# Kernel optimization log

Hardware: AMD Instinct MI355X
Metric: run time of the kernel (lower is better)

The kernel has to match this reference:

```python
import jax, jax.numpy as jnp
import numpy as np

N = 50000      # nodes
E = 800000     # edges (avg degree 16)
IN = 256       # input feature dim
HID = 128      # hidden dim
H = 4          # heads
C = HID // H   # per-head dim = 32
L = 3          # layers


def setup_inputs() -> dict:
    key = jax.random.key(0)
    ks = jax.random.split(key, 16)
    s = 0.02
    f32 = jnp.float32
    inp = {
        "x": jax.random.normal(ks[0], (N, IN), f32),
        "edge_index": jax.random.randint(ks[1], (2, E), 0, N, dtype=jnp.int32),
        "edge_attr": jax.random.normal(ks[2], (E, 1), f32),
        "Wi": jax.random.normal(ks[3], (IN, HID), f32) * s,
        "bi": jnp.zeros((HID,), f32),
        "Wq": jax.random.normal(ks[4], (L, HID, HID), f32) * s,
        "bq": jnp.zeros((L, HID), f32),
        "Wk": jax.random.normal(ks[5], (L, HID, HID), f32) * s,
        "bk": jnp.zeros((L, HID), f32),
        "Wv": jax.random.normal(ks[6], (L, HID, HID), f32) * s,
        "bv": jnp.zeros((L, HID), f32),
        "We": jax.random.normal(ks[7], (L, 1, HID), f32) * s,      # lin_edge, no bias
        "Wskip": jax.random.normal(ks[8], (L, HID, HID), f32) * s,
        "bskip": jnp.zeros((L, HID), f32),
        "Wbeta": jax.random.normal(ks[9], (L, 3 * HID, 1), f32) * s,  # lin_beta, no bias
        "ln_g": jnp.ones((L, HID), f32),
        "ln_b": jnp.zeros((L, HID), f32),
    }
    return inp


def _layer_norm(x, g, b, eps=1e-5):
    mu = jnp.mean(x, axis=-1, keepdims=True)
    var = jnp.var(x, axis=-1, keepdims=True)
    return (x - mu) * jax.lax.rsqrt(var + eps) * g + b


def _transformer_conv(h, src, dst, edge_attr, Wq, bq, Wk, bk, Wv, bv, We, Wskip, bskip, Wbeta):
    # node-level projections [N, HID]
    q = h @ Wq + bq
    k = h @ Wk + bk
    v = h @ Wv + bv
    e = edge_attr @ We                       # [E, HID] edge embedding
    # per-edge gathered features [E, H, C]
    qi = q[dst].reshape(E, H, C)
    kj = (k[src] + e).reshape(E, H, C)
    vj = (v[src] + e).reshape(E, H, C)
    # attention logits [E, H]
    alpha = jnp.sum(qi * kj, axis=-1) / np.sqrt(C)
    # segment softmax over destination node
    amax = jax.ops.segment_max(alpha, dst, num_segments=N)   # [N, H]
    ex = jnp.exp(alpha - amax[dst])
    denom = jax.ops.segment_sum(ex, dst, num_segments=N)     # [N, H]
    attn = ex / (denom[dst] + 1e-16)                         # [E, H]
    # scatter-add aggregation -> [N, H, C] -> concat heads [N, HID]
    out = jax.ops.segment_sum(attn[..., None] * vj, dst, num_segments=N).reshape(N, HID)
    # gated skip (beta=True, root_weight=True)
    x_r = h @ Wskip + bskip
    beta = jax.nn.sigmoid(jnp.concatenate([out, x_r, out - x_r], axis=-1) @ Wbeta)  # [N, 1]
    return beta * x_r + (1.0 - beta) * out


def reference(x, edge_index, edge_attr, Wi, bi, Wq, bq, Wk, bk, Wv, bv, We, Wskip, bskip, Wbeta, ln_g, ln_b):
    src = edge_index[0]
    dst = edge_index[1]
    h = x @ Wi + bi
    for l in range(L):
        res = h
        h = _transformer_conv(h, src, dst, edge_attr,
                              Wq[l], bq[l], Wk[l], bk[l], Wv[l], bv[l],
                              We[l], Wskip[l], bskip[l], Wbeta[l])
        h = jax.nn.gelu(h, approximate=False)
        h = _layer_norm(h + res, ln_g[l], ln_b[l])
        # dropout: eval mode -> identity
    return h
```

## Files before the change

kernel.cpp:

```cpp
#include <hip/hip_runtime.h>
#include <math.h>

#define NNODES 50000
#define NEDGES 800000
#define DIN 256
#define DHID 128

typedef __attribute__((ext_vector_type(8))) short short8;
typedef __attribute__((ext_vector_type(4))) float f32x4;
typedef __attribute__((ext_vector_type(2))) float f32x2;

__device__ __forceinline__ unsigned short f2bf(float f) {
    unsigned u = __builtin_bit_cast(unsigned, f);
    u += 0x7fffu + ((u >> 16) & 1u);
    return (unsigned short)(u >> 16);
}
__device__ __forceinline__ float bf2f(unsigned short s) {
    return __builtin_bit_cast(float, (unsigned)s << 16);
}
__device__ __forceinline__ unsigned packbf(float a, float b) {
    return (unsigned)f2bf(a) | ((unsigned)f2bf(b) << 16);
}

__global__ __launch_bounds__(256) void k_hist(const int* __restrict__ dst, int* __restrict__ counts) {
    int e = blockIdx.x * 256 + threadIdx.x;
    if (e < NEDGES) atomicAdd(&counts[dst[e]], 1);
}

__global__ __launch_bounds__(256) void k_scan_block(const int* __restrict__ in, int* __restrict__ out,
                                                    int* __restrict__ partials, int n) {
    __shared__ int sh[256];
    int tid = threadIdx.x;
    int i = blockIdx.x * 256 + tid;
    int vv = (i < n) ? in[i] : 0;
    sh[tid] = vv;
    __syncthreads();
    for (int off = 1; off < 256; off <<= 1) {
        int t = (tid >= off) ? sh[tid - off] : 0;
        __syncthreads();
        sh[tid] += t;
        __syncthreads();
    }
    if (i < n) out[i] = sh[tid];
    if (tid == 255) partials[blockIdx.x] = sh[255];
}

__global__ __launch_bounds__(256) void k_scan_partials(int* __restrict__ partials, int nb) {
    __shared__ int sh[256];
    int tid = threadIdx.x;
    int vv = (tid < nb) ? partials[tid] : 0;
    sh[tid] = vv;
    __syncthreads();
    for (int off = 1; off < 256; off <<= 1) {
        int t = (tid >= off) ? sh[tid - off] : 0;
        __syncthreads();
        sh[tid] += t;
        __syncthreads();
    }
    if (tid < nb) partials[tid] = sh[tid];
}

__global__ __launch_bounds__(256) void k_apply(const int* __restrict__ partials, int* __restrict__ row_ptr, int n) {
    int i = blockIdx.x * 256 + threadIdx.x;
    if (i < n) {
        int add = blockIdx.x ? partials[blockIdx.x - 1] : 0;
        row_ptr[i + 1] += add;
    }
    if (i == 0) row_ptr[0] = 0;
}

__global__ __launch_bounds__(256) void k_scatter(const int* __restrict__ src, const int* __restrict__ dst,
                                                 const float* __restrict__ ea, const int* __restrict__ row_ptr,
                                                 int* __restrict__ fill, int2* __restrict__ esrc) {
    int e = blockIdx.x * 256 + threadIdx.x;
    if (e < NEDGES) {
        int d = dst[e];
        int old = atomicSub(&fill[d], 1);
        int pos = row_ptr[d] + old - 1;
        esrc[pos] = make_int2(src[e], __float_as_int(ea[e]));
    }
}

__global__ __launch_bounds__(256) void prep_w(const float* __restrict__ Wi, const float* __restrict__ Wq,
                                              const float* __restrict__ Wk, const float* __restrict__ Wv,
                                              const float* __restrict__ Ws, unsigned short* __restrict__ Wit,
                                              unsigned short* __restrict__ Wt3) {
    int idx = blockIdx.x * 256 + threadIdx.x;
    if (idx < DHID * DIN) {
        int n = idx >> 8, kk = idx & 255;
        Wit[idx] = f2bf(Wi[kk * DHID + n]);
    }
    int idx2 = idx - DHID * DIN;
    if (idx2 >= 0 && idx2 < 3 * 512 * DHID) {
        int l = idx2 / (512 * DHID);
        int rem = idx2 - l * 512 * DHID;
        int r = rem >> 7;
        int kk = rem & 127;
        int sel = r >> 7, rl = r & 127;
        const float* srcm = sel == 0 ? Wq : sel == 1 ? Wk : sel == 2 ? Wv : Ws;
        Wt3[idx2] = f2bf(srcm[l * DHID * DHID + kk * DHID + rl]);
    }
}

__global__ __launch_bounds__(256) void gemm_in(const float* __restrict__ A, const unsigned short* __restrict__ Wt,
                                               const float* __restrict__ bias, unsigned* __restrict__ h32, int M) {
    __shared__ short As[128 * 128];
    const int tid = threadIdx.x;
    const int lane = tid & 63;
    const int wid = tid >> 6;
    const int row0 = blockIdx.x * 128;
    const int wr = (wid & 1) * 64;
    const int wc = (wid >> 1) * 64;
    f32x4 acc[4][4] = {};
    const int srow = tid >> 1;
    const int sk = (tid & 1) * 64;
    const int grow = min(row0 + srow, M - 1);
    for (int kt = 0; kt < 2; ++kt) {
        const float* ap = A + (size_t)grow * DIN + kt * 128 + sk;
#pragma unroll
        for (int i = 0; i < 8; ++i) {
            float4 f0 = *(const float4*)(ap + i * 8);
            float4 f1 = *(const float4*)(ap + i * 8 + 4);
            short8 s;
            s[0] = f2bf(f0.x); s[1] = f2bf(f0.y); s[2] = f2bf(f0.z); s[3] = f2bf(f0.w);
            s[4] = f2bf(f1.x); s[5] = f2bf(f1.y); s[6] = f2bf(f1.z); s[7] = f2bf(f1.w);
            int g = (sk >> 3) + i;
            *(short8*)(&As[srow * 128 + ((g ^ (srow & 7)) << 3)]) = s;
        }
        __syncthreads();
#pragma unroll
        for (int ks = 0; ks < 4; ++ks) {
            short8 a[4], b[4];
#pragma unroll
            for (int m = 0; m < 4; ++m) {
                int r = wr + m * 16 + (lane & 15);
                int g = ks * 4 + (lane >> 4);
                a[m] = *(const short8*)(&As[r * 128 + ((g ^ (r & 7)) << 3)]);
            }
#pragma unroll
            for (int n = 0; n < 4; ++n) {
                int c = wc + n * 16 + (lane & 15);
                b[n] = *(const short8*)(Wt + (size_t)c * DIN + kt * 128 + ks * 32 + (lane >> 4) * 8);
            }
#pragma unroll
            for (int m = 0; m < 4; ++m)
#pragma unroll
                for (int n = 0; n < 4; ++n)
                    acc[m][n] = __builtin_amdgcn_mfma_f32_16x16x32_bf16(a[m], b[n], acc[m][n], 0, 0, 0);
        }
        __syncthreads();
    }
    float* my = ((float*)As) + wid * 1024;
    float bb[4];
#pragma unroll
    for (int n = 0; n < 4; ++n) bb[n] = bias[wc + n * 16 + (lane & 15)];
    const int rr = lane >> 2;
    const int cb = lane & 3;
#pragma unroll
    for (int m = 0; m < 4; ++m) {
#pragma unroll
        for (int n = 0; n < 4; ++n) {
            int lc = n * 16 + (lane & 15);
#pragma unroll
            for (int j = 0; j < 4; ++j) {
                int row = (lane >> 4) * 4 + j;
                my[row * 64 + (((lc >> 2) ^ (row & 7)) << 2) + (lc & 3)] = acc[m][n][j] + bb[n];
            }
        }
        float vals[16];
#pragma unroll
        for (int s = 0; s < 4; ++s) {
            int gx = (cb * 4 + s) ^ (rr & 7);
            f32x4 t4 = *(const f32x4*)(my + rr * 64 + gx * 4);
            vals[s * 4 + 0] = t4.x; vals[s * 4 + 1] = t4.y; vals[s * 4 + 2] = t4.z; vals[s * 4 + 3] = t4.w;
        }
        int grow2 = row0 + wr + m * 16 + rr;
        if (grow2 < M) {
            unsigned pk[8];
#pragma unroll
            for (int d = 0; d < 8; ++d) pk[d] = packbf(vals[2 * d], vals[2 * d + 1]);
            unsigned* op = h32 + (size_t)grow2 * 64 + (wc >> 1) + cb * 8;
            *(uint4*)op = make_uint4(pk[0], pk[1], pk[2], pk[3]);
            *(uint4*)(op + 4) = make_uint4(pk[4], pk[5], pk[6], pk[7]);
        }
    }
}

__global__ __launch_bounds__(512) void gemm_qkvs(const unsigned short* __restrict__ A,
                                                 const unsigned short* __restrict__ Wt, const float* __restrict__ bq,
                                                 const float* __restrict__ bk, const float* __restrict__ bv,
                                                 const float* __restrict__ bs, unsigned* __restrict__ q32,
                                                 unsigned* __restrict__ kv, unsigned* __restrict__ xr32, int M) {
    __shared__ short As[128 * 128];
    const int tid = threadIdx.x;
    const int lane = tid & 63;
    const int wid = tid >> 6;
    const int row0 = blockIdx.x * 128;
    const int sel = wid >> 2;
    const int wr = (wid & 1) * 64;
    const int wc = ((wid >> 1) & 1) * 64;
    f32x4 acc0[4][4] = {}, acc1[4][4] = {};
    {
        const int srow = tid >> 2;
        const int sk = (tid & 3) * 32;
        const int grow = min(row0 + srow, M - 1);
        const unsigned short* ap = A + (size_t)grow * DHID + sk;
#pragma unroll
        for (int i = 0; i < 4; ++i) {
            short8 s = *(const short8*)(ap + i * 8);
            int g = (sk >> 3) + i;
            *(short8*)(&As[srow * 128 + ((g ^ (srow & 7)) << 3)]) = s;
        }
    }
    __syncthreads();
    const int b0base = sel ? 128 : 0;
    const int b1base = sel ? 256 : 384;
#pragma unroll
    for (int ks = 0; ks < 4; ++ks) {
        short8 a[4], b0[4], b1[4];
#pragma unroll
        for (int m = 0; m < 4; ++m) {
            int r = wr + m * 16 + (lane & 15);
            int g = ks * 4 + (lane >> 4);
            a[m] = *(const short8*)(&As[r * 128 + ((g ^ (r & 7)) << 3)]);
        }
#pragma unroll
        for (int n = 0; n < 4; ++n) {
            int rb = wc + n * 16 + (lane & 15);
            b0[n] = *(const short8*)(Wt + (size_t)(b0base + rb) * DHID + ks * 32 + (lane >> 4) * 8);
            b1[n] = *(const short8*)(Wt + (size_t)(b1base + rb) * DHID + ks * 32 + (lane >> 4) * 8);
        }
#pragma unroll
        for (int m = 0; m < 4; ++m)
#pragma unroll
            for (int n = 0; n < 4; ++n) {
                acc0[m][n] = __builtin_amdgcn_mfma_f32_16x16x32_bf16(a[m], b0[n], acc0[m][n], 0, 0, 0);
                acc1[m][n] = __builtin_amdgcn_mfma_f32_16x16x32_bf16(a[m], b1[n], acc1[m][n], 0, 0, 0);
            }
    }
    __syncthreads();
    float* my = ((float*)As) + wid * 1024;
    const float* bias0 = sel ? bk : bq;
    const float* bias1 = sel ? bv : bs;
    float bb0[4], bb1[4];
#pragma unroll
    for (int n = 0; n < 4; ++n) {
        int c = wc + n * 16 + (lane & 15);
        bb0[n] = bias0[c];
        bb1[n] = bias1[c];
    }
    const int rr = lane >> 2;
    const int cb = lane & 3;
#pragma unroll
    for (int m = 0; m < 4; ++m) {
        float vals0[16], vals1[16];
#pragma unroll
        for (int n = 0; n < 4; ++n) {
            int lc = n * 16 + (lane & 15);
#pragma unroll
            for (int j = 0; j < 4; ++j) {
                int row = (lane >> 4) * 4 + j;
                my[row * 64 + (((lc >> 2) ^ (row & 7)) << 2) + (lc & 3)] = acc0[m][n][j] + bb0[n];
            }
        }
#pragma unroll
        for (int s = 0; s < 4; ++s) {
            int gx = (cb * 4 + s) ^ (rr & 7);
            f32x4 t4 = *(const f32x4*)(my + rr * 64 + gx * 4);
            vals0[s * 4 + 0] = t4.x; vals0[s * 4 + 1] = t4.y; vals0[s * 4 + 2] = t4.z; vals0[s * 4 + 3] = t4.w;
        }
#pragma unroll
        for (int n = 0; n < 4; ++n) {
            int lc = n * 16 + (lane & 15);
#pragma unroll
            for (int j = 0; j < 4; ++j) {
                int row = (lane >> 4) * 4 + j;
                my[row * 64 + (((lc >> 2) ^ (row & 7)) << 2) + (lc & 3)] = acc1[m][n][j] + bb1[n];
            }
        }
#pragma unroll
        for (int s = 0; s < 4; ++s) {
            int gx = (cb * 4 + s) ^ (rr & 7);
            f32x4 t4 = *(const f32x4*)(my + rr * 64 + gx * 4);
            vals1[s * 4 + 0] = t4.x; vals1[s * 4 + 1] = t4.y; vals1[s * 4 + 2] = t4.z; vals1[s * 4 + 3] = t4.w;
        }
        int grow2 = row0 + wr + m * 16 + rr;
        if (grow2 < M) {
            size_t obase = (size_t)grow2 * 64 + (wc >> 1) + cb * 8;
            if (sel == 0) {
                unsigned p0[8], p1[8];
#pragma unroll
                for (int d = 0; d < 8; ++d) {
                    p0[d] = packbf(vals0[2 * d], vals0[2 * d + 1]);
                    p1[d] = packbf(vals1[2 * d], vals1[2 * d + 1]);
                }
                *(uint4*)(q32 + obase) = make_uint4(p0[0], p0[1], p0[2], p0[3]);
                *(uint4*)(q32 + obase + 4) = make_uint4(p0[4], p0[5], p0[6], p0[7]);
                *(uint4*)(xr32 + obase) = make_uint4(p1[0], p1[1], p1[2], p1[3]);
                *(uint4*)(xr32 + obase + 4) = make_uint4(p1[4], p1[5], p1[6], p1[7]);
            } else {
                unsigned pk[8];
#pragma unroll
                for (int d = 0; d < 8; ++d) {
                    unsigned u = (unsigned)__builtin_amdgcn_cvt_pk_fp8_f32(vals0[2 * d], vals0[2 * d + 1], 0, false);
                    u = (unsigned)__builtin_amdgcn_cvt_pk_fp8_f32(vals1[2 * d], vals1[2 * d + 1], (int)u, true);
                    pk[d] = u;
                }
                *(uint4*)(kv + obase) = make_uint4(pk[0], pk[1], pk[2], pk[3]);
                *(uint4*)(kv + obase + 4) = make_uint4(pk[4], pk[5], pk[6], pk[7]);
            }
        }
    }
}

__global__ __launch_bounds__(256) void node_attn_fuse(const unsigned* __restrict__ q32,
                                                      const unsigned* __restrict__ kv, const int2* __restrict__ esrc,
                                                      const float* __restrict__ We, const int* __restrict__ row_ptr,
                                                      const unsigned* __restrict__ xr32, const unsigned* res32,
                                                      const float* __restrict__ Wb, const float* __restrict__ lng,
                                                      const float* __restrict__ lnb, unsigned* houtb, float* houtf) {
    __shared__ float sh_o[4][128];
    const int tid = threadIdx.x;
    const int wv = tid >> 6;
    const int lane = tid & 63;
    const int wid = blockIdx.x * 4 + wv;
    if (wid >= NNODES) return;
    const int ln = lane & 15;
    const int g = lane >> 4;
    const int base = row_ptr[wid], end = row_ptr[wid + 1];
    const float SC = 0.25505654047688565f;
    const float THR = 8.0f;

    float qv[8], wev[8];
    {
        uint4 qw = *(const uint4*)(q32 + (size_t)wid * 64 + 4 * ln);
#pragma unroll
        for (int t = 0; t < 4; ++t) {
            unsigned u = ((const unsigned*)&qw)[t];
            qv[2 * t] = bf2f((unsigned short)u) * SC;
            qv[2 * t + 1] = bf2f((unsigned short)(u >> 16)) * SC;
        }
        float4 wlo = *(const float4*)(We + 8 * ln);
        float4 whi = *(const float4*)(We + 8 * ln + 4);
        wev[0] = wlo.x; wev[1] = wlo.y; wev[2] = wlo.z; wev[3] = wlo.w;
        wev[4] = whi.x; wev[5] = whi.y; wev[6] = whi.z; wev[7] = whi.w;
    }
    float qwe = 0.f;
#pragma unroll
    for (int i = 0; i < 8; ++i) qwe = fmaf(qv[i], wev[i], qwe);
    qwe += __shfl_xor(qwe, 1);
    qwe += __shfl_xor(qwe, 2);

    float m = -1e30f, sden = 0.f, tacc = 0.f;
    float acc[8] = {};
    const unsigned* kvp = kv + 4 * ln;

    for (int cbse = base; cbse < end; cbse += 64) {
        int cnt = min(end - cbse, 64);
        int s_l = 0;
        float a_l = 0.f;
        if (lane < cnt) {
            int2 sa = esrc[cbse + lane];
            s_l = sa.x;
            a_l = __int_as_float(sa.y);
        }
        int jmax = (cnt + 3) >> 2;
        for (int j = 0; j < jmax; ++j) {
            int slot = j * 4 + g;
            bool valid = slot < cnt;
            int sN = __shfl(s_l, slot);
            float av = __shfl(a_l, slot);
            if (!valid) sN = 0;
            uint4 kvw = *(const uint4*)(kvp + (size_t)sN * 64);
            float vj[8];
            float p = 0.f;
#pragma unroll
            for (int t = 0; t < 4; ++t) {
                unsigned u = ((const unsigned*)&kvw)[t];
                f32x2 kk = __builtin_amdgcn_cvt_pk_f32_fp8((int)u, false);
                f32x2 vv = __builtin_amdgcn_cvt_pk_f32_fp8((int)u, true);
                p = fmaf(qv[2 * t], kk.x, p);
                p = fmaf(qv[2 * t + 1], kk.y, p);
                vj[2 * t] = vv.x;
                vj[2 * t + 1] = vv.y;
            }
            p += __shfl_xor(p, 1);
            p += __shfl_xor(p, 2);
            p = fmaf(av, qwe, p);
            p = valid ? p : -3e38f;
            if (__all(p - m <= THR)) {
                float wgt = exp2f(p - m);
                sden += wgt;
                tacc = fmaf(wgt, av, tacc);
#pragma unroll
                for (int i = 0; i < 8; ++i) acc[i] = fmaf(wgt, vj[i], acc[i]);
            } else {
                float mn = fmaxf(m, p);
                float wgt = exp2f(p - mn);
                float sc = exp2f(m - mn);
                sden = fmaf(sden, sc, wgt);
                tacc = fmaf(tacc, sc, wgt * av);
#pragma unroll
                for (int i = 0; i < 8; ++i) acc[i] = fmaf(acc[i], sc, wgt * vj[i]);
                m = mn;
            }
        }
    }

#pragma unroll
    for (int off = 16; off <= 32; off <<= 1) {
        float m_o = __shfl_xor(m, off);
        float sden_o = __shfl_xor(sden, off);
        float t_o = __shfl_xor(tacc, off);
        float mn = fmaxf(m, m_o);
        float sa = exp2f(m - mn), sb = exp2f(m_o - mn);
        sden = sden * sa + sden_o * sb;
        tacc = tacc * sa + t_o * sb;
#pragma unroll
        for (int i = 0; i < 8; ++i) acc[i] = acc[i] * sa + __shfl_xor(acc[i], off) * sb;
        m = mn;
    }
    float rden = 1.f / (sden + 1e-16f);
    if (g == 0) {
#pragma unroll
        for (int i = 0; i < 8; ++i) sh_o[wv][8 * ln + i] = fmaf(tacc, wev[i], acc[i]) * rden;
    }
    __asm__ volatile("s_waitcnt lgkmcnt(0)" ::: "memory");

    const int c0 = 2 * lane;
    const float2 ov0v = *(const float2*)(&sh_o[wv][c0]);
    float o0 = ov0v.x, o1 = ov0v.y;
    const unsigned xw = xr32[(size_t)wid * 64 + lane];
    const float x0 = bf2f((unsigned short)xw), x1 = bf2f((unsigned short)(xw >> 16));
    const float2 w0 = *(const float2*)(Wb + c0);
    const float2 w1 = *(const float2*)(Wb + 128 + c0);
    const float2 w2 = *(const float2*)(Wb + 256 + c0);
    float bl = o0 * w0.x + o1 * w0.y + x0 * w1.x + x1 * w1.y + (o0 - x0) * w2.x + (o1 - x1) * w2.y;
#pragma unroll
    for (int off = 32; off; off >>= 1) bl += __shfl_xor(bl, off);
    float beta = 1.f / (1.f + __expf(-bl));
    float g0 = beta * x0 + (1.f - beta) * o0;
    float g1 = beta * x1 + (1.f - beta) * o1;
    g0 = 0.5f * g0 * (1.f + erff(g0 * 0.70710678118654752f));
    g1 = 0.5f * g1 * (1.f + erff(g1 * 0.70710678118654752f));
    const unsigned rw = res32[(size_t)wid * 64 + lane];
    float t0 = g0 + bf2f((unsigned short)rw);
    float t1 = g1 + bf2f((unsigned short)(rw >> 16));
    float su = t0 + t1, sq = t0 * t0 + t1 * t1;
#pragma unroll
    for (int off = 32; off; off >>= 1) {
        su += __shfl_xor(su, off);
        sq += __shfl_xor(sq, off);
    }
    float mu = su * (1.f / 128.f);
    float var = sq * (1.f / 128.f) - mu * mu;
    float inv = rsqrtf(var + 1e-5f);
    const float2 gv = *(const float2*)(lng + c0);
    const float2 bv2 = *(const float2*)(lnb + c0);
    float ovx = (t0 - mu) * inv * gv.x + bv2.x;
    float ovy = (t1 - mu) * inv * gv.y + bv2.y;
    if (houtf) {
        *(float2*)(houtf + (size_t)wid * 128 + c0) = make_float2(ovx, ovy);
    } else {
        houtb[(size_t)wid * 64 + lane] = packbf(ovx, ovy);
    }
}

extern "C" void kernel_launch(void* const* d_in, const int* in_sizes, int n_in, void* d_out, int out_size,
                              void* d_ws, size_t ws_size, hipStream_t stream) {
    const float* x = (const float*)d_in[0];
    const int* ei = (const int*)d_in[1];
    const float* ea = (const float*)d_in[2];
    const float* Wi = (const float*)d_in[3];
    const float* bi = (const float*)d_in[4];
    const float* Wq = (const float*)d_in[5];
    const float* bq = (const float*)d_in[6];
    const float* Wk = (const float*)d_in[7];
    const float* bk = (const float*)d_in[8];
    const float* Wv = (const float*)d_in[9];
    const float* bv = (const float*)d_in[10];
    const float* We = (const float*)d_in[11];
    const float* Wskip = (const float*)d_in[12];
    const float* bskip = (const float*)d_in[13];
    const float* Wbeta = (const float*)d_in[14];
    const float* lng = (const float*)d_in[15];
    const float* lnb = (const float*)d_in[16];

    const int* srcp = ei;
    const int* dstp = ei + NEDGES;

    char* p = (char*)d_ws;
    auto alloc = [&](size_t bytes) {
        void* r = (void*)p;
        p += (bytes + 255) & ~(size_t)255;
        return r;
    };
    unsigned* h32 = (unsigned*)alloc((size_t)NNODES * 64 * 4);
    unsigned* q32 = (unsigned*)alloc((size_t)NNODES * 64 * 4);
    unsigned* xr32 = (unsigned*)alloc((size_t)NNODES * 64 * 4);
    unsigned* kv = (unsigned*)alloc((size_t)NNODES * 64 * 4);
    unsigned short* Wit = (unsigned short*)alloc((size_t)DHID * DIN * 2);
    unsigned short* Wt3 = (unsigned short*)alloc((size_t)3 * 512 * DHID * 2);
    int* counts = (int*)alloc((size_t)NNODES * 4);
    int* row_ptr = (int*)alloc((size_t)(NNODES + 1) * 4);
    int2* esrc = (int2*)alloc((size_t)NEDGES * 8);
    int* partials = (int*)alloc(256 * 4);

    const int EB = (NEDGES + 255) / 256;
    const int NB = (NNODES + 255) / 256;
    const int GB = (NNODES + 127) / 128;
    const int WB = (NNODES + 3) / 4;
    const int PB = (DHID * DIN + 3 * 512 * DHID + 255) / 256;

    prep_w<<<PB, 256, 0, stream>>>(Wi, Wq, Wk, Wv, Wskip, Wit, Wt3);

    hipMemsetAsync(counts, 0, (size_t)NNODES * 4, stream);
    k_hist<<<EB, 256, 0, stream>>>(dstp, counts);
    k_scan_block<<<NB, 256, 0, stream>>>(counts, row_ptr + 1, partials, NNODES);
    k_scan_partials<<<1, 256, 0, stream>>>(partials, NB);
    k_apply<<<NB, 256, 0, stream>>>(partials, row_ptr, NNODES);
    k_scatter<<<EB, 256, 0, stream>>>(srcp, dstp, ea, row_ptr, counts, esrc);

    gemm_in<<<GB, 256, 0, stream>>>(x, Wit, bi, h32, NNODES);

    for (int l = 0; l < 3; ++l) {
        const size_t bo = (size_t)l * 128;
        gemm_qkvs<<<GB, 512, 0, stream>>>((const unsigned short*)h32, Wt3 + (size_t)l * 512 * DHID, bq + bo, bk + bo,
                                          bv + bo, bskip + bo, q32, kv, xr32, NNODES);
        node_attn_fuse<<<WB, 256, 0, stream>>>(q32, kv, esrc, We + bo, row_ptr, xr32, h32,
                                               Wbeta + (size_t)l * 384, lng + bo, lnb + bo, h32,
                                               (l == 2) ? (float*)d_out : nullptr);
    }
}
```

Before: 376.2 us.

## Process 8 edges per wave with prefetched KV rows and DPP reductions

The attention kernel now assigns 8 lanes per edge, so each lane handles 16 channels and the wave covers 8 edges per iteration instead of 4. Edge metadata is staged in shared memory, and the next edge's KV row is prefetched one iteration ahead to hide gather latency. Cross-lane reductions use DPP moves in place of some shuffles. The separate partial-scan kernel is folded into the apply kernel, which drops one launch. The trade-off is more registers per lane (16 accumulators plus prefetch buffers), which may lower occupancy, and low-degree nodes waste more lanes per iteration.

```diff
diff --git a/kernel.cpp b/kernel.cpp
--- a/kernel.cpp
+++ b/kernel.cpp
@@ -20,6 +20,12 @@
 }
 __device__ __forceinline__ unsigned packbf(float a, float b) {
     return (unsigned)f2bf(a) | ((unsigned)f2bf(b) << 16);
+}
+__device__ __forceinline__ float dpp_xor1(float x) {
+    return __builtin_bit_cast(float, __builtin_amdgcn_update_dpp(0, __builtin_bit_cast(int, x), 0xB1, 0xF, 0xF, true));
+}
+__device__ __forceinline__ float dpp_xor8(float x) {
+    return __builtin_bit_cast(float, __builtin_amdgcn_update_dpp(0, __builtin_bit_cast(int, x), 0x128, 0xF, 0xF, true));
 }
 
 __global__ __launch_bounds__(256) void k_hist(const int* __restrict__ dst, int* __restrict__ counts) {
@@ -45,7 +51,8 @@
     if (tid == 255) partials[blockIdx.x] = sh[255];
 }
 
-__global__ __launch_bounds__(256) void k_scan_partials(int* __restrict__ partials, int nb) {
+__global__ __launch_bounds__(256) void k_apply2(const int* __restrict__ partials, int* __restrict__ row_ptr, int n,
+                                                int nb) {
     __shared__ int sh[256];
     int tid = threadIdx.x;
     int vv = (tid < nb) ? partials[tid] : 0;
@@ -57,13 +64,9 @@
         sh[tid] += t;
         __syncthreads();
     }
-    if (tid < nb) partials[tid] = sh[tid];
-}
-
-__global__ __launch_bounds__(256) void k_apply(const int* __restrict__ partials, int* __restrict__ row_ptr, int n) {
-    int i = blockIdx.x * 256 + threadIdx.x;
+    int i = blockIdx.x * 256 + tid;
     if (i < n) {
-        int add = blockIdx.x ? partials[blockIdx.x - 1] : 0;
+        int add = blockIdx.x ? sh[blockIdx.x - 1] : 0;
         row_ptr[i + 1] += add;
     }
     if (i == 0) row_ptr[0] = 0;
@@ -320,72 +323,81 @@
                                                       const float* __restrict__ Wb, const float* __restrict__ lng,
                                                       const float* __restrict__ lnb, unsigned* houtb, float* houtf) {
     __shared__ float sh_o[4][128];
+    __shared__ int2 sh_meta[4][64];
     const int tid = threadIdx.x;
     const int wv = tid >> 6;
     const int lane = tid & 63;
     const int wid = blockIdx.x * 4 + wv;
     if (wid >= NNODES) return;
-    const int ln = lane & 15;
-    const int g = lane >> 4;
+    const int ln = lane & 7;
+    const int g = lane >> 3;
     const int base = row_ptr[wid], end = row_ptr[wid + 1];
     const float SC = 0.25505654047688565f;
     const float THR = 8.0f;
 
-    float qv[8], wev[8];
+    float qv[16];
     {
-        uint4 qw = *(const uint4*)(q32 + (size_t)wid * 64 + 4 * ln);
+        uint4 qa = *(const uint4*)(q32 + (size_t)wid * 64 + 8 * ln);
+        uint4 qb = *(const uint4*)(q32 + (size_t)wid * 64 + 8 * ln + 4);
+        unsigned qd[8] = {qa.x, qa.y, qa.z, qa.w, qb.x, qb.y, qb.z, qb.w};
+#pragma unroll
+        for (int t = 0; t < 8; ++t) {
+            qv[2 * t] = bf2f((unsigned short)qd[t]) * SC;
+            qv[2 * t + 1] = bf2f((unsigned short)(qd[t] >> 16)) * SC;
+        }
+    }
+    float qwe;
+    {
+        float s = 0.f;
 #pragma unroll
         for (int t = 0; t < 4; ++t) {
-            unsigned u = ((const unsigned*)&qw)[t];
-            qv[2 * t] = bf2f((unsigned short)u) * SC;
-            qv[2 * t + 1] = bf2f((unsigned short)(u >> 16)) * SC;
-        }
-        float4 wlo = *(const float4*)(We + 8 * ln);
-        float4 whi = *(const float4*)(We + 8 * ln + 4);
-        wev[0] = wlo.x; wev[1] = wlo.y; wev[2] = wlo.z; wev[3] = wlo.w;
-        wev[4] = whi.x; wev[5] = whi.y; wev[6] = whi.z; wev[7] = whi.w;
-    }
-    float qwe = 0.f;
-#pragma unroll
-    for (int i = 0; i < 8; ++i) qwe = fmaf(qv[i], wev[i], qwe);
-    qwe += __shfl_xor(qwe, 1);
-    qwe += __shfl_xor(qwe, 2);
+            float4 w4 = *(const float4*)(We + 16 * ln + 4 * t);
+            s = fmaf(qv[4 * t], w4.x, s);
+            s = fmaf(qv[4 * t + 1], w4.y, s);
+            s = fmaf(qv[4 * t + 2], w4.z, s);
+            s = fmaf(qv[4 * t + 3], w4.w, s);
+        }
+        qwe = s + dpp_xor1(s);
+    }
 
     float m = -1e30f, sden = 0.f, tacc = 0.f;
-    float acc[8] = {};
-    const unsigned* kvp = kv + 4 * ln;
+    float acc[16] = {};
+    const unsigned* kvp = kv + 8 * ln;
 
     for (int cbse = base; cbse < end; cbse += 64) {
         int cnt = min(end - cbse, 64);
-        int s_l = 0;
-        float a_l = 0.f;
-        if (lane < cnt) {
-            int2 sa = esrc[cbse + lane];
-            s_l = sa.x;
-            a_l = __int_as_float(sa.y);
-        }
-        int jmax = (cnt + 3) >> 2;
+        int2 me = (lane < cnt) ? esrc[cbse + lane] : make_int2(0, 0);
+        sh_meta[wv][lane] = me;
+        __asm__ volatile("s_waitcnt lgkmcnt(0)" ::: "memory");
+        int jmax = (cnt + 7) >> 3;
+        int2 mc = sh_meta[wv][g];
+        const unsigned* rowp = kvp + (size_t)mc.x * 64;
+        uint4 ka = *(const uint4*)rowp;
+        uint4 kb = *(const uint4*)(rowp + 4);
         for (int j = 0; j < jmax; ++j) {
-            int slot = j * 4 + g;
-            bool valid = slot < cnt;
-            int sN = __shfl(s_l, slot);
-            float av = __shfl(a_l, slot);
-            if (!valid) sN = 0;
-            uint4 kvw = *(const uint4*)(kvp + (size_t)sN * 64);
-            float vj[8];
+            bool more = (j + 1 < jmax);
+            int2 mn_ = sh_meta[wv][(((j + 1) << 3) + g) & 63];
+            uint4 ka1 = ka, kb1 = kb;
+            if (more) {
+                const unsigned* rowp1 = kvp + (size_t)mn_.x * 64;
+                ka1 = *(const uint4*)rowp1;
+                kb1 = *(const uint4*)(rowp1 + 4);
+            }
+            bool valid = ((j << 3) + g) < cnt;
+            float av = __int_as_float(mc.y);
+            unsigned kd[8] = {ka.x, ka.y, ka.z, ka.w, kb.x, kb.y, kb.z, kb.w};
+            float vj[16];
             float p = 0.f;
 #pragma unroll
-            for (int t = 0; t < 4; ++t) {
-                unsigned u = ((const unsigned*)&kvw)[t];
-                f32x2 kk = __builtin_amdgcn_cvt_pk_f32_fp8((int)u, false);
-                f32x2 vv = __builtin_amdgcn_cvt_pk_f32_fp8((int)u, true);
+            for (int t = 0; t < 8; ++t) {
+                f32x2 kk = __builtin_amdgcn_cvt_pk_f32_fp8((int)kd[t], false);
+                f32x2 vvv = __builtin_amdgcn_cvt_pk_f32_fp8((int)kd[t], true);
                 p = fmaf(qv[2 * t], kk.x, p);
                 p = fmaf(qv[2 * t + 1], kk.y, p);
-                vj[2 * t] = vv.x;
-                vj[2 * t + 1] = vv.y;
-            }
-            p += __shfl_xor(p, 1);
-            p += __shfl_xor(p, 2);
+                vj[2 * t] = vvv.x;
+                vj[2 * t + 1] = vvv.y;
+            }
+            p += dpp_xor1(p);
             p = fmaf(av, qwe, p);
             p = valid ? p : -3e38f;
             if (__all(p - m <= THR)) {
@@ -393,37 +405,58 @@
                 sden += wgt;
                 tacc = fmaf(wgt, av, tacc);
 #pragma unroll
-                for (int i = 0; i < 8; ++i) acc[i] = fmaf(wgt, vj[i], acc[i]);
+                for (int i = 0; i < 16; ++i) acc[i] = fmaf(wgt, vj[i], acc[i]);
             } else {
-                float mn = fmaxf(m, p);
-                float wgt = exp2f(p - mn);
-                float sc = exp2f(m - mn);
+                float mn2 = fmaxf(m, p);
+                float wgt = exp2f(p - mn2);
+                float sc = exp2f(m - mn2);
                 sden = fmaf(sden, sc, wgt);
                 tacc = fmaf(tacc, sc, wgt * av);
 #pragma unroll
-                for (int i = 0; i < 8; ++i) acc[i] = fmaf(acc[i], sc, wgt * vj[i]);
-                m = mn;
-            }
-        }
-    }
-
+                for (int i = 0; i < 16; ++i) acc[i] = fmaf(acc[i], sc, wgt * vj[i]);
+                m = mn2;
+            }
+            mc = mn_;
+            ka = ka1;
+            kb = kb1;
+        }
+    }
+
+    {
+        float m_o = dpp_xor8(m), s_o = dpp_xor8(sden), t_o = dpp_xor8(tacc);
+        float mn2 = fmaxf(m, m_o);
+        float sa = exp2f(m - mn2), sb = exp2f(m_o - mn2);
+        sden = sden * sa + s_o * sb;
+        tacc = tacc * sa + t_o * sb;
+#pragma unroll
+        for (int i = 0; i < 16; ++i) acc[i] = acc[i] * sa + dpp_xor8(acc[i]) * sb;
+        m = mn2;
+    }
 #pragma unroll
     for (int off = 16; off <= 32; off <<= 1) {
         float m_o = __shfl_xor(m, off);
-        float sden_o = __shfl_xor(sden, off);
+        float s_o = __shfl_xor(sden, off);
         float t_o = __shfl_xor(tacc, off);
-        float mn = fmaxf(m, m_o);
-        float sa = exp2f(m - mn), sb = exp2f(m_o - mn);
-        sden = sden * sa + sden_o * sb;
+        float mn2 = fmaxf(m, m_o);
+        float sa = exp2f(m - mn2), sb = exp2f(m_o - mn2);
+        sden = sden * sa + s_o * sb;
         tacc = tacc * sa + t_o * sb;
 #pragma unroll
-        for (int i = 0; i < 8; ++i) acc[i] = acc[i] * sa + __shfl_xor(acc[i], off) * sb;
-        m = mn;
+        for (int i = 0; i < 16; ++i) acc[i] = acc[i] * sa + __shfl_xor(acc[i], off) * sb;
+        m = mn2;
     }
     float rden = 1.f / (sden + 1e-16f);
     if (g == 0) {
 #pragma unroll
-        for (int i = 0; i < 8; ++i) sh_o[wv][8 * ln + i] = fmaf(tacc, wev[i], acc[i]) * rden;
+        for (int t = 0; t < 4; ++t) {
+            float4 w4 = *(const float4*)(We + 16 * ln + 4 * t);
+            float4 o4;
+            o4.x = fmaf(tacc, w4.x, acc[4 * t]) * rden;
+            o4.y = fmaf(tacc, w4.y, acc[4 * t + 1]) * rden;
+            o4.z = fmaf(tacc, w4.z, acc[4 * t + 2]) * rden;
+            o4.w = fmaf(tacc, w4.w, acc[4 * t + 3]) * rden;
+            *(float4*)(&sh_o[wv][16 * ln + 4 * t]) = o4;
+        }
     }
     __asm__ volatile("s_waitcnt lgkmcnt(0)" ::: "memory");
 
@@ -517,8 +550,7 @@
     hipMemsetAsync(counts, 0, (size_t)NNODES * 4, stream);
     k_hist<<<EB, 256, 0, stream>>>(dstp, counts);
     k_scan_block<<<NB, 256, 0, stream>>>(counts, row_ptr + 1, partials, NNODES);
-    k_scan_partials<<<1, 256, 0, stream>>>(partials, NB);
-    k_apply<<<NB, 256, 0, stream>>>(partials, row_ptr, NNODES);
+    k_apply2<<<NB, 256, 0, stream>>>(partials, row_ptr, NNODES, NB);
     k_scatter<<<EB, 256, 0, stream>>>(srcp, dstp, ea, row_ptr, counts, esrc);
 
     gemm_in<<<GB, 256, 0, stream>>>(x, Wit, bi, h32, NNODES);
```

Measured after the change: 422.3 us. 12.3% more time.

## Process one node per 16-lane group in attention kernel with DPP reductions

Applied to the files above, without the earlier changes.

The fused attention kernel changes from one node per 64-lane wavefront (four edge slots across lane groups, merged at the end through shuffles and shared memory) to one node per 16-lane group, so each wavefront handles four nodes and walks their edges serially. The next edge's source row is prefetched during the current edge's work, cross-lane sums use DPP row operations instead of shuffles, and the epilogue works on eight features per lane with vector loads and stores. Separately, the partial-sum scan is folded into the apply kernel, removing one launch. Because all four nodes in a wave iterate up to the largest degree among them, degree imbalance can leave lanes idle, in exchange for removing the cross-group merge and shared-memory step.

```diff
diff --git a/kernel.cpp b/kernel.cpp
--- a/kernel.cpp
+++ b/kernel.cpp
@@ -20,6 +20,25 @@
 }
 __device__ __forceinline__ unsigned packbf(float a, float b) {
     return (unsigned)f2bf(a) | ((unsigned)f2bf(b) << 16);
+}
+__device__ __forceinline__ float dpp_xor1(float x) {
+    return __builtin_bit_cast(float, __builtin_amdgcn_update_dpp(0, __builtin_bit_cast(int, x), 0xB1, 0xF, 0xF, true));
+}
+__device__ __forceinline__ float dpp_xor2(float x) {
+    return __builtin_bit_cast(float, __builtin_amdgcn_update_dpp(0, __builtin_bit_cast(int, x), 0x4E, 0xF, 0xF, true));
+}
+__device__ __forceinline__ float dpp_hmirror(float x) {
+    return __builtin_bit_cast(float, __builtin_amdgcn_update_dpp(0, __builtin_bit_cast(int, x), 0x141, 0xF, 0xF, true));
+}
+__device__ __forceinline__ float dpp_mirror(float x) {
+    return __builtin_bit_cast(float, __builtin_amdgcn_update_dpp(0, __builtin_bit_cast(int, x), 0x140, 0xF, 0xF, true));
+}
+__device__ __forceinline__ float red16(float x) {
+    x += dpp_xor1(x);
+    x += dpp_xor2(x);
+    x += dpp_hmirror(x);
+    x += dpp_mirror(x);
+    return x;
 }
 
 __global__ __launch_bounds__(256) void k_hist(const int* __restrict__ dst, int* __restrict__ counts) {
@@ -45,7 +64,8 @@
     if (tid == 255) partials[blockIdx.x] = sh[255];
 }
 
-__global__ __launch_bounds__(256) void k_scan_partials(int* __restrict__ partials, int nb) {
+__global__ __launch_bounds__(256) void k_apply2(const int* __restrict__ partials, int* __restrict__ row_ptr, int n,
+                                                int nb) {
     __shared__ int sh[256];
     int tid = threadIdx.x;
     int vv = (tid < nb) ? partials[tid] : 0;
@@ -57,13 +77,9 @@
         sh[tid] += t;
         __syncthreads();
     }
-    if (tid < nb) partials[tid] = sh[tid];
-}
-
-__global__ __launch_bounds__(256) void k_apply(const int* __restrict__ partials, int* __restrict__ row_ptr, int n) {
-    int i = blockIdx.x * 256 + threadIdx.x;
+    int i = blockIdx.x * 256 + tid;
     if (i < n) {
-        int add = blockIdx.x ? partials[blockIdx.x - 1] : 0;
+        int add = blockIdx.x ? sh[blockIdx.x - 1] : 0;
         row_ptr[i + 1] += add;
     }
     if (i == 0) row_ptr[0] = 0;
@@ -319,150 +335,174 @@
                                                       const unsigned* __restrict__ xr32, const unsigned* res32,
                                                       const float* __restrict__ Wb, const float* __restrict__ lng,
                                                       const float* __restrict__ lnb, unsigned* houtb, float* houtf) {
-    __shared__ float sh_o[4][128];
     const int tid = threadIdx.x;
-    const int wv = tid >> 6;
     const int lane = tid & 63;
-    const int wid = blockIdx.x * 4 + wv;
-    if (wid >= NNODES) return;
-    const int ln = lane & 15;
-    const int g = lane >> 4;
-    const int base = row_ptr[wid], end = row_ptr[wid + 1];
+    const int lnl = lane & 15;
+    const int gbase = lane & 48;
+    const int node = blockIdx.x * 16 + (tid >> 4);
+    const int base = row_ptr[node], end = row_ptr[node + 1];
     const float SC = 0.25505654047688565f;
     const float THR = 8.0f;
 
     float qv[8], wev[8];
     {
-        uint4 qw = *(const uint4*)(q32 + (size_t)wid * 64 + 4 * ln);
+        uint4 qw = *(const uint4*)(q32 + (size_t)node * 64 + 4 * lnl);
+        unsigned qd[4] = {qw.x, qw.y, qw.z, qw.w};
 #pragma unroll
         for (int t = 0; t < 4; ++t) {
-            unsigned u = ((const unsigned*)&qw)[t];
-            qv[2 * t] = bf2f((unsigned short)u) * SC;
-            qv[2 * t + 1] = bf2f((unsigned short)(u >> 16)) * SC;
-        }
-        float4 wlo = *(const float4*)(We + 8 * ln);
-        float4 whi = *(const float4*)(We + 8 * ln + 4);
+            qv[2 * t] = bf2f((unsigned short)qd[t]) * SC;
+            qv[2 * t + 1] = bf2f((unsigned short)(qd[t] >> 16)) * SC;
+        }
+        float4 wlo = *(const float4*)(We + 8 * lnl);
+        float4 whi = *(const float4*)(We + 8 * lnl + 4);
         wev[0] = wlo.x; wev[1] = wlo.y; wev[2] = wlo.z; wev[3] = wlo.w;
         wev[4] = whi.x; wev[5] = whi.y; wev[6] = whi.z; wev[7] = whi.w;
     }
-    float qwe = 0.f;
-#pragma unroll
-    for (int i = 0; i < 8; ++i) qwe = fmaf(qv[i], wev[i], qwe);
-    qwe += __shfl_xor(qwe, 1);
-    qwe += __shfl_xor(qwe, 2);
+    float qwe;
+    {
+        float s = 0.f;
+#pragma unroll
+        for (int i = 0; i < 8; ++i) s = fmaf(qv[i], wev[i], s);
+        s += dpp_xor1(s);
+        s += dpp_xor2(s);
+        qwe = s;
+    }
 
     float m = -1e30f, sden = 0.f, tacc = 0.f;
     float acc[8] = {};
-    const unsigned* kvp = kv + 4 * ln;
-
-    for (int cbse = base; cbse < end; cbse += 64) {
-        int cnt = min(end - cbse, 64);
+    const unsigned* kvp = kv + 4 * lnl;
+
+    for (int off = 0; ; off += 16) {
+        int cnt = min(end - base - off, 16);
+        if (__all(cnt <= 0)) break;
         int s_l = 0;
         float a_l = 0.f;
-        if (lane < cnt) {
-            int2 sa = esrc[cbse + lane];
+        if (lnl < cnt) {
+            int2 sa = esrc[base + off + lnl];
             s_l = sa.x;
             a_l = __int_as_float(sa.y);
         }
-        int jmax = (cnt + 3) >> 2;
-        for (int j = 0; j < jmax; ++j) {
-            int slot = j * 4 + g;
-            bool valid = slot < cnt;
-            int sN = __shfl(s_l, slot);
-            float av = __shfl(a_l, slot);
-            if (!valid) sN = 0;
-            uint4 kvw = *(const uint4*)(kvp + (size_t)sN * 64);
+        int cm = max(cnt, 0);
+        cm = max(cm, __shfl_xor(cm, 16));
+        cm = max(cm, __shfl_xor(cm, 32));
+        int src_n = __shfl(s_l, gbase);
+        float av_n = __shfl(a_l, gbase);
+        uint4 kw_n = *(const uint4*)(kvp + (size_t)src_n * 64);
+        for (int j = 0; j < cm; ++j) {
+            uint4 kw = kw_n;
+            float av = av_n;
+            bool valid = j < cnt;
+            if (j + 1 < cm) {
+                int src1 = __shfl(s_l, gbase + j + 1);
+                av_n = __shfl(a_l, gbase + j + 1);
+                kw_n = *(const uint4*)(kvp + (size_t)src1 * 64);
+            }
+            unsigned kd[4] = {kw.x, kw.y, kw.z, kw.w};
             float vj[8];
             float p = 0.f;
 #pragma unroll
             for (int t = 0; t < 4; ++t) {
-                unsigned u = ((const unsigned*)&kvw)[t];
-                f32x2 kk = __builtin_amdgcn_cvt_pk_f32_fp8((int)u, false);
-                f32x2 vv = __builtin_amdgcn_cvt_pk_f32_fp8((int)u, true);
+                f32x2 kk = __builtin_amdgcn_cvt_pk_f32_fp8((int)kd[t], false);
+                f32x2 vv = __builtin_amdgcn_cvt_pk_f32_fp8((int)kd[t], true);
                 p = fmaf(qv[2 * t], kk.x, p);
                 p = fmaf(qv[2 * t + 1], kk.y, p);
                 vj[2 * t] = vv.x;
                 vj[2 * t + 1] = vv.y;
             }
-            p += __shfl_xor(p, 1);
-            p += __shfl_xor(p, 2);
+            p += dpp_xor1(p);
+            p += dpp_xor2(p);
             p = fmaf(av, qwe, p);
             p = valid ? p : -3e38f;
-            if (__all(p - m <= THR)) {
+            if (__any(p - m > THR)) {
+                float mn2 = fmaxf(m, p);
+                float wgt = exp2f(p - mn2);
+                float sc = exp2f(m - mn2);
+                sden = fmaf(sden, sc, wgt);
+                tacc = fmaf(tacc, sc, wgt * av);
+#pragma unroll
+                for (int i = 0; i < 8; ++i) acc[i] = fmaf(acc[i], sc, wgt * vj[i]);
+                m = mn2;
+            } else {
                 float wgt = exp2f(p - m);
                 sden += wgt;
                 tacc = fmaf(wgt, av, tacc);
 #pragma unroll
                 for (int i = 0; i < 8; ++i) acc[i] = fmaf(wgt, vj[i], acc[i]);
-            } else {
-                float mn = fmaxf(m, p);
-                float wgt = exp2f(p - mn);
-                float sc = exp2f(m - mn);
-                sden = fmaf(sden, sc, wgt);
-                tacc = fmaf(tacc, sc, wgt * av);
-#pragma unroll
-                for (int i = 0; i < 8; ++i) acc[i] = fmaf(acc[i], sc, wgt * vj[i]);
-                m = mn;
-            }
-        }
-    }
-
-#pragma unroll
-    for (int off = 16; off <= 32; off <<= 1) {
-        float m_o = __shfl_xor(m, off);
-        float sden_o = __shfl_xor(sden, off);
-        float t_o = __shfl_xor(tacc, off);
-        float mn = fmaxf(m, m_o);
-        float sa = exp2f(m - mn), sb = exp2f(m_o - mn);
-        sden = sden * sa + sden_o * sb;
-        tacc = tacc * sa + t_o * sb;
-#pragma unroll
-        for (int i = 0; i < 8; ++i) acc[i] = acc[i] * sa + __shfl_xor(acc[i], off) * sb;
-        m = mn;
-    }
+            }
+        }
+    }
+
     float rden = 1.f / (sden + 1e-16f);
-    if (g == 0) {
-#pragma unroll
-        for (int i = 0; i < 8; ++i) sh_o[wv][8 * ln + i] = fmaf(tacc, wev[i], acc[i]) * rden;
-    }
-    __asm__ volatile("s_waitcnt lgkmcnt(0)" ::: "memory");
-
-    const int c0 = 2 * lane;
-    const float2 ov0v = *(const float2*)(&sh_o[wv][c0]);
-    float o0 = ov0v.x, o1 = ov0v.y;
-    const unsigned xw = xr32[(size_t)wid * 64 + lane];
-    const float x0 = bf2f((unsigned short)xw), x1 = bf2f((unsigned short)(xw >> 16));
-    const float2 w0 = *(const float2*)(Wb + c0);
-    const float2 w1 = *(const float2*)(Wb + 128 + c0);
-    const float2 w2 = *(const float2*)(Wb + 256 + c0);
-    float bl = o0 * w0.x + o1 * w0.y + x0 * w1.x + x1 * w1.y + (o0 - x0) * w2.x + (o1 - x1) * w2.y;
-#pragma unroll
-    for (int off = 32; off; off >>= 1) bl += __shfl_xor(bl, off);
+    float o[8];
+#pragma unroll
+    for (int i = 0; i < 8; ++i) o[i] = fmaf(tacc, wev[i], acc[i]) * rden;
+
+    float x[8];
+    {
+        uint4 xw = *(const uint4*)(xr32 + (size_t)node * 64 + 4 * lnl);
+        unsigned xd[4] = {xw.x, xw.y, xw.z, xw.w};
+#pragma unroll
+        for (int t = 0; t < 4; ++t) {
+            x[2 * t] = bf2f((unsigned short)xd[t]);
+            x[2 * t + 1] = bf2f((unsigned short)(xd[t] >> 16));
+        }
+    }
+    float bl = 0.f;
+#pragma unroll
+    for (int t = 0; t < 2; ++t) {
+        float4 w0 = *(const float4*)(Wb + 8 * lnl + 4 * t);
+        float4 w1 = *(const float4*)(Wb + 128 + 8 * lnl + 4 * t);
+        float4 w2 = *(const float4*)(Wb + 256 + 8 * lnl + 4 * t);
+        bl = fmaf(o[4 * t], w0.x, bl); bl = fmaf(o[4 * t + 1], w0.y, bl);
+        bl = fmaf(o[4 * t + 2], w0.z, bl); bl = fmaf(o[4 * t + 3], w0.w, bl);
+        bl = fmaf(x[4 * t], w1.x, bl); bl = fmaf(x[4 * t + 1], w1.y, bl);
+        bl = fmaf(x[4 * t + 2], w1.z, bl); bl = fmaf(x[4 * t + 3], w1.w, bl);
+        bl = fmaf(o[4 * t] - x[4 * t], w2.x, bl); bl = fmaf(o[4 * t + 1] - x[4 * t + 1], w2.y, bl);
+        bl = fmaf(o[4 * t + 2] - x[4 * t + 2], w2.z, bl); bl = fmaf(o[4 * t + 3] - x[4 * t + 3], w2.w, bl);
+    }
+    bl = red16(bl);
     float beta = 1.f / (1.f + __expf(-bl));
-    float g0 = beta * x0 + (1.f - beta) * o0;
-    float g1 = beta * x1 + (1.f - beta) * o1;
-    g0 = 0.5f * g0 * (1.f + erff(g0 * 0.70710678118654752f));
-    g1 = 0.5f * g1 * (1.f + erff(g1 * 0.70710678118654752f));
-    const unsigned rw = res32[(size_t)wid * 64 + lane];
-    float t0 = g0 + bf2f((unsigned short)rw);
-    float t1 = g1 + bf2f((unsigned short)(rw >> 16));
-    float su = t0 + t1, sq = t0 * t0 + t1 * t1;
-#pragma unroll
-    for (int off = 32; off; off >>= 1) {
-        su += __shfl_xor(su, off);
-        sq += __shfl_xor(sq, off);
-    }
+    float tpre[8];
+    {
+        uint4 rw = *(const uint4*)(res32 + (size_t)node * 64 + 4 * lnl);
+        unsigned rd[4] = {rw.x, rw.y, rw.z, rw.w};
+#pragma unroll
+        for (int i = 0; i < 8; ++i) {
+            float gg = beta * x[i] + (1.f - beta) * o[i];
+            gg = 0.5f * gg * (1.f + erff(gg * 0.70710678118654752f));
+            float rv = (i & 1) ? bf2f((unsigned short)(rd[i >> 1] >> 16)) : bf2f((unsigned short)rd[i >> 1]);
+            tpre[i] = gg + rv;
+        }
+    }
+    float su = 0.f, sq = 0.f;
+#pragma unroll
+    for (int i = 0; i < 8; ++i) {
+        su += tpre[i];
+        sq = fmaf(tpre[i], tpre[i], sq);
+    }
+    su = red16(su);
+    sq = red16(sq);
     float mu = su * (1.f / 128.f);
     float var = sq * (1.f / 128.f) - mu * mu;
     float inv = rsqrtf(var + 1e-5f);
-    const float2 gv = *(const float2*)(lng + c0);
-    const float2 bv2 = *(const float2*)(lnb + c0);
-    float ovx = (t0 - mu) * inv * gv.x + bv2.x;
-    float ovy = (t1 - mu) * inv * gv.y + bv2.y;
+    float4 g0 = *(const float4*)(lng + 8 * lnl);
+    float4 g1 = *(const float4*)(lng + 8 * lnl + 4);
+    float4 b0 = *(const float4*)(lnb + 8 * lnl);
+    float4 b1 = *(const float4*)(lnb + 8 * lnl + 4);
+    float gg[8] = {g0.x, g0.y, g0.z, g0.w, g1.x, g1.y, g1.z, g1.w};
+    float bb[8] = {b0.x, b0.y, b0.z, b0.w, b1.x, b1.y, b1.z, b1.w};
+    float ov[8];
+#pragma unroll
+    for (int i = 0; i < 8; ++i) ov[i] = (tpre[i] - mu) * inv * gg[i] + bb[i];
     if (houtf) {
-        *(float2*)(houtf + (size_t)wid * 128 + c0) = make_float2(ovx, ovy);
+        float* op = houtf + (size_t)node * 128 + 8 * lnl;
+        *(float4*)op = make_float4(ov[0], ov[1], ov[2], ov[3]);
+        *(float4*)(op + 4) = make_float4(ov[4], ov[5], ov[6], ov[7]);
     } else {
-        houtb[(size_t)wid * 64 + lane] = packbf(ovx, ovy);
+        unsigned pk[4];
+#pragma unroll
+        for (int d = 0; d < 4; ++d) pk[d] = packbf(ov[2 * d], ov[2 * d + 1]);
+        *(uint4*)(houtb + (size_t)node * 64 + 4 * lnl) = make_uint4(pk[0], pk[1], pk[2], pk[3]);
     }
 }
 
@@ -509,7 +549,7 @@
     const int EB = (NEDGES + 255) / 256;
     const int NB = (NNODES + 255) / 256;
     const int GB = (NNODES + 127) / 128;
-    const int WB = (NNODES + 3) / 4;
+    const int WB = NNODES / 16;
     const int PB = (DHID * DIN + 3 * 512 * DHID + 255) / 256;
 
     prep_w<<<PB, 256, 0, stream>>>(Wi, Wq, Wk, Wv, Wskip, Wit, Wt3);
@@ -517,8 +557,7 @@
     hipMemsetAsync(counts, 0, (size_t)NNODES * 4, stream);
     k_hist<<<EB, 256, 0, stream>>>(dstp, counts);
     k_scan_block<<<NB, 256, 0, stream>>>(counts, row_ptr + 1, partials, NNODES);
-    k_scan_partials<<<1, 256, 0, stream>>>(partials, NB);
-    k_apply<<<NB, 256, 0, stream>>>(partials, row_ptr, NNODES);
+    k_apply2<<<NB, 256, 0, stream>>>(partials, row_ptr, NNODES, NB);
     k_scatter<<<EB, 256, 0, stream>>>(srcp, dstp, ea, row_ptr, counts, esrc);
 
     gemm_in<<<GB, 256, 0, stream>>>(x, Wit, bi, h32, NNODES);
```

New measurement: 330.4 us. 12.2% less time.
